# Optimization experiments

Hardware: AMD Instinct MI355X
Metric: run time of the kernel (lower is better)

Reference implementation:

```python
import jax, jax.numpy as jnp
import numpy as np

OUT_FEATURES = 16384
IN_FEATURES = 4096


def setup_inputs() -> dict:
    key = jax.random.key(0)
    k1, k2, k3, k4 = jax.random.split(key, 4)
    # activations [B, S, in]
    x = jax.random.normal(k1, (4, 2048, IN_FEATURES), dtype=jnp.float32)
    # packed int4 weights: two nibbles per uint8, total out*in values (even, no pad)
    n_packed = OUT_FEATURES * IN_FEATURES // 2
    weight_packed = jax.random.randint(k2, (n_packed,), 0, 256, dtype=jnp.int32).astype(jnp.uint8)
    # per-row dequant scale [out, 1], positive like abs-max/7
    scale = jax.random.uniform(k3, (OUT_FEATURES, 1), dtype=jnp.float32, minval=1e-3, maxval=0.05)
    bias = jax.random.normal(k4, (OUT_FEATURES,), dtype=jnp.float32) * 0.01
    return {"x": x, "weight_packed": weight_packed, "scale": scale, "bias": bias}


def reference(x, weight_packed, scale, bias):
    # unpack: even positions = low nibble, odd positions = high nibble
    low = (weight_packed & 15).astype(jnp.int8)
    high = ((weight_packed >> 4) & 15).astype(jnp.int8)
    q = jnp.stack([low, high], axis=-1).reshape(-1)  # interleave -> [out*in]
    # sign-extend 4-bit two's complement: values >7 map to negative
    q = jnp.where(q > 7, q - 16, q)
    # dequantize with per-row scale -> [out, in]
    w = q.reshape(OUT_FEATURES, IN_FEATURES).astype(jnp.float32) * scale
    # F.linear: y = x @ w.T + bias
    return jnp.einsum('bsi,oi->bso', x, w) + bias
```

## Files before the change

### kernel.cpp

```cpp
#include <hip/hip_runtime.h>
#include <hip/hip_bf16.h>
#include <stdint.h>

typedef short short8 __attribute__((ext_vector_type(8)));
typedef float floatx4 __attribute__((ext_vector_type(4)));

static constexpr int KTOT = 4096;
static constexpr int NTOT = 16384;
static constexpr int MTOT = 8192;

#define GLOAD_LDS16(g, l)                                              \
  __builtin_amdgcn_global_load_lds(                                    \
      (const __attribute__((address_space(1))) void*)(g),              \
      (__attribute__((address_space(3))) void*)(l), 16, 0, 0)

__device__ __forceinline__ uint32_t pack2_bf16_rne(float lo, float hi) {
  uint32_t a = __builtin_bit_cast(uint32_t, lo);
  uint32_t b = __builtin_bit_cast(uint32_t, hi);
  a += 0x7FFFu + ((a >> 16) & 1u);
  b += 0x7FFFu + ((b >> 16) & 1u);
  return __builtin_amdgcn_perm(b, a, 0x07060302u);
}


__global__ __launch_bounds__(256) void cvt_x_kernel(
    const float* __restrict__ X, ushort* __restrict__ Xb) {
  const size_t i = (size_t)blockIdx.x * 256 + threadIdx.x;
  const float4 a = *reinterpret_cast<const float4*>(X + i * 8);
  const float4 b = *reinterpret_cast<const float4*>(X + i * 8 + 4);
  uint4 o;
  o.x = pack2_bf16_rne(a.x, a.y);
  o.y = pack2_bf16_rne(a.z, a.w);
  o.z = pack2_bf16_rne(b.x, b.y);
  o.w = pack2_bf16_rne(b.z, b.w);
  *reinterpret_cast<uint4*>(Xb + i * 8) = o;
}

__global__ __launch_bounds__(256) void cvt_w_kernel(
    const uint32_t* __restrict__ Wp, ushort* __restrict__ Wb) {
  const size_t i = (size_t)blockIdx.x * 256 + threadIdx.x;
  const uint4 w = *reinterpret_cast<const uint4*>(Wp + i * 4);
  const uint32_t wd[4] = {w.x, w.y, w.z, w.w};
  uint4 o;
  uint32_t* op = reinterpret_cast<uint32_t*>(&o);
  #pragma unroll
  for (int p = 0; p < 4; ++p) {
    int v0 = ((int)(wd[p] << 28)) >> 28;
    int v1 = ((int)(wd[p] << 24)) >> 28;
    uint32_t f0 = __builtin_bit_cast(uint32_t, (float)v0);
    uint32_t f1 = __builtin_bit_cast(uint32_t, (float)v1);
    op[p] = __builtin_amdgcn_perm(f1, f0, 0x07060302u);
  }
  *reinterpret_cast<uint4*>(Wb + i * 8) = o;
}


static constexpr int BM = 256, BN = 256, BK = 32;
static constexpr int NT = KTOT / BK;

#define READ_FRAGS(AF0, AF1, BF, buf)                                   \
  {                                                                     \
    const ushort* Ab_ = As + (buf) * 8192 + abase + laneoff;            \
    const ushort* Bb_ = Bs + (buf) * 8192 + bbase + laneoff;            \
    _Pragma("unroll")                                                   \
    for (int n = 0; n < 4; ++n)                                         \
      BF[n] = *reinterpret_cast<const short8*>(Bb_ + n * 512);          \
    _Pragma("unroll")                                                   \
    for (int m = 0; m < 4; ++m)                                         \
      AF0[m] = *reinterpret_cast<const short8*>(Ab_ + m * 512);         \
    _Pragma("unroll")                                                   \
    for (int m = 0; m < 4; ++m)                                         \
      AF1[m] = *reinterpret_cast<const short8*>(Ab_ + (m + 4) * 512);   \
  }

#define STAGE(st_)                                                      \
  if ((st_) < NT) {                                                     \
    const int sb_ = (st_) & 3;                                          \
    const size_t kof_ = (size_t)(st_) * BK;                             \
    GLOAD_LDS16(agA + kof_,           aldsw + sb_ * 8192);              \
    GLOAD_LDS16(agA + kof_ + rowstep, aldsw + sb_ * 8192 + 4096);       \
    GLOAD_LDS16(agB + kof_,           bldsw + sb_ * 8192);              \
    GLOAD_LDS16(agB + kof_ + rowstep, bldsw + sb_ * 8192 + 4096);       \
  }

#define MFMA_CLUSTER(AF0, AF1, BF)                                      \
  __builtin_amdgcn_s_setprio(1);                                        \
  _Pragma("unroll")                                                     \
  for (int m = 0; m < 4; ++m)                                           \
    _Pragma("unroll")                                                   \
    for (int n = 0; n < 4; ++n)                                         \
      acc[m][n] = __builtin_amdgcn_mfma_f32_16x16x32_bf16(AF0[m], BF[n], acc[m][n], 0, 0, 0); \
  _Pragma("unroll")                                                     \
  for (int m = 0; m < 4; ++m)                                           \
    _Pragma("unroll")                                                   \
    for (int n = 0; n < 4; ++n)                                         \
      acc[m + 4][n] = __builtin_amdgcn_mfma_f32_16x16x32_bf16(AF1[m], BF[n], acc[m + 4][n], 0, 0, 0); \
  __builtin_amdgcn_s_setprio(0);

#define BOUNDARY(k_)                                                    \
  if ((k_) + 3 < NT) { asm volatile("s_waitcnt vmcnt(4)\ns_barrier" ::: "memory"); } \
  else               { asm volatile("s_waitcnt vmcnt(0)\ns_barrier" ::: "memory"); }

__global__ __launch_bounds__(512, 2) void gemm_bf16_256_kernel(
    const ushort* __restrict__ Xb,
    const ushort* __restrict__ Wb,
    const float* __restrict__ scale,
    const float* __restrict__ bias,
    float* __restrict__ Y)
{
  __shared__ ushort As[4 * 8192];
  __shared__ ushort Bs[4 * 8192];

  const int t    = threadIdx.x;
  const int lane = t & 63;
  const int wv   = t >> 6;
  const int wr   = wv >> 2;
  const int wcn  = wv & 3;

  const int wg  = blockIdx.x;
  const int xcd = wg & 7;
  const int s   = wg >> 3;
  const int bm0 = (xcd * 4 + (s & 3)) * BM;
  const int bn0 = (s >> 2) * BN;

  const int clg  = (t & 7) ^ ((t >> 3) & 7);
  const int srow = ((t >> 3) << 1) | (clg >> 2);
  const int scol = (clg & 3) * 8;
  const ushort* agA = Xb + (size_t)(bm0 + srow) * KTOT + scol;
  const ushort* agB = Wb + (size_t)(bn0 + srow) * KTOT + scol;
  const size_t rowstep = (size_t)128 * KTOT;
  ushort* aldsw = As + wv * 512;
  ushort* bldsw = Bs + wv * 512;

  const int p    = lane >> 4;
  const int l15  = lane & 15;
  const int cph  = (((l15 & 1) << 2) | p) ^ ((l15 >> 1) & 7);
  const int laneoff = (l15 >> 1) * 64 + cph * 8;
  const int abase = wr * 4096;
  const int bbase = wcn * 2048;

  floatx4 acc[8][4];
  #pragma unroll
  for (int m = 0; m < 8; ++m)
    #pragma unroll
    for (int n = 0; n < 4; ++n)
      acc[m][n] = (floatx4){0.f, 0.f, 0.f, 0.f};

  #pragma unroll
  for (int pt = 0; pt < 3; ++pt) {
    const size_t kof = (size_t)pt * BK;
    GLOAD_LDS16(agA + kof,           aldsw + pt * 8192);
    GLOAD_LDS16(agA + kof + rowstep, aldsw + pt * 8192 + 4096);
    GLOAD_LDS16(agB + kof,           bldsw + pt * 8192);
    GLOAD_LDS16(agB + kof + rowstep, bldsw + pt * 8192 + 4096);
  }
  asm volatile("s_waitcnt vmcnt(4)\ns_barrier" ::: "memory");

  short8 a0A[4], a1A[4], bA[4];
  short8 a0B[4], a1B[4], bB[4];
  READ_FRAGS(a0A, a1A, bA, 0);

  for (int kt = 0; kt < NT; kt += 2) {
    READ_FRAGS(a0B, a1B, bB, (kt + 1) & 3);
    STAGE(kt + 3);
    MFMA_CLUSTER(a0A, a1A, bA);
    BOUNDARY(kt);

    if (kt + 2 < NT) { READ_FRAGS(a0A, a1A, bA, (kt + 2) & 3); }
    STAGE(kt + 4);
    MFMA_CLUSTER(a0B, a1B, bB);
    if (kt + 2 < NT) { BOUNDARY(kt + 1); }
  }

  const int crow = (lane >> 4) * 4;
  const int ccol = lane & 15;
  #pragma unroll
  for (int n = 0; n < 4; ++n) {
    const int col  = bn0 + wcn * 64 + n * 16 + ccol;
    const float sc = scale[col];
    const float bz = bias[col];
    #pragma unroll
    for (int m = 0; m < 8; ++m) {
      const int row0 = bm0 + wr * 128 + m * 16 + crow;
      float* yp = Y + (size_t)row0 * NTOT + col;
      #pragma unroll
      for (int r = 0; r < 4; ++r)
        yp[(size_t)r * NTOT] = acc[m][n][r] * sc + bz;
    }
  }
}


static constexpr int FBM = 128, FBN = 128, FBK = 64;
static constexpr int LDSS = 72;
static constexpr int FNSTEP = KTOT / FBK;

__global__ __launch_bounds__(256) void int4_linear_fused_kernel(
    const float* __restrict__ X,
    const uint32_t* __restrict__ Wp,
    const float* __restrict__ scale,
    const float* __restrict__ bias,
    float* __restrict__ Y)
{
  __shared__ ushort As[FBM * LDSS];
  __shared__ ushort Bs[FBN * LDSS];

  const int t    = threadIdx.x;
  const int lane = t & 63;
  const int wv   = t >> 6;
  const int wr   = wv >> 1;
  const int wc   = wv & 1;
  const int bm0 = blockIdx.y * FBM;
  const int bn0 = blockIdx.x * FBN;
  const int srow = t >> 1;
  const int sh   = t & 1;

  const float*    ag = X  + (size_t)(bm0 + srow) * KTOT + sh * 32;
  const uint32_t* bg = Wp + (size_t)(bn0 + srow) * (KTOT / 2) + sh * 16;

  float4 areg[8];
  uint4  breg[4];
  #pragma unroll
  for (int j = 0; j < 8; ++j) areg[j] = *reinterpret_cast<const float4*>(ag + j * 4);
  #pragma unroll
  for (int j = 0; j < 4; ++j) breg[j] = *reinterpret_cast<const uint4*>(bg + j * 4);

  floatx4 acc[4][4];
  #pragma unroll
  for (int m = 0; m < 4; ++m)
    #pragma unroll
    for (int n = 0; n < 4; ++n)
      acc[m][n] = (floatx4){0.f, 0.f, 0.f, 0.f};

  ushort* adst = &As[srow * LDSS + sh * 32];
  ushort* bdst = &Bs[srow * LDSS + sh * 32];

  for (int ks = 0; ks < FNSTEP; ++ks) {
    {
      uint32_t ab[16];
      #pragma unroll
      for (int j = 0; j < 8; ++j) {
        uint32_t u0 = __builtin_bit_cast(uint32_t, areg[j].x) + 0x8000u;
        uint32_t u1 = __builtin_bit_cast(uint32_t, areg[j].y) + 0x8000u;
        uint32_t u2 = __builtin_bit_cast(uint32_t, areg[j].z) + 0x8000u;
        uint32_t u3 = __builtin_bit_cast(uint32_t, areg[j].w) + 0x8000u;
        ab[2*j]   = __builtin_amdgcn_perm(u1, u0, 0x07060302u);
        ab[2*j+1] = __builtin_amdgcn_perm(u3, u2, 0x07060302u);
      }
      uint32_t bb[16];
      #pragma unroll
      for (int j = 0; j < 4; ++j) {
        const uint32_t wq[4] = {breg[j].x, breg[j].y, breg[j].z, breg[j].w};
        #pragma unroll
        for (int p2 = 0; p2 < 4; ++p2) {
          const uint32_t w = wq[p2];
          int v0 = ((int)(w << 28)) >> 28;
          int v1 = ((int)(w << 24)) >> 28;
          uint32_t f0 = __builtin_bit_cast(uint32_t, (float)v0);
          uint32_t f1 = __builtin_bit_cast(uint32_t, (float)v1);
          bb[j*4 + p2] = __builtin_amdgcn_perm(f1, f0, 0x07060302u);
        }
      }
      #pragma unroll
      for (int j = 0; j < 4; ++j) {
        *reinterpret_cast<uint4*>(adst + j * 8) = *reinterpret_cast<const uint4*>(&ab[j*4]);
        *reinterpret_cast<uint4*>(bdst + j * 8) = *reinterpret_cast<const uint4*>(&bb[j*4]);
      }
    }
    __syncthreads();

    if (ks + 1 < FNSTEP) {
      const float*    ap = ag + (ks + 1) * FBK;
      const uint32_t* bp = bg + (ks + 1) * (FBK / 2);
      #pragma unroll
      for (int j = 0; j < 8; ++j) areg[j] = *reinterpret_cast<const float4*>(ap + j * 4);
      #pragma unroll
      for (int j = 0; j < 4; ++j) breg[j] = *reinterpret_cast<const uint4*>(bp + j * 4);
    }

    #pragma unroll
    for (int kk = 0; kk < 2; ++kk) {
      const int ko = kk * 32 + (lane >> 4) * 8;
      short8 af[4], bf[4];
      #pragma unroll
      for (int m = 0; m < 4; ++m)
        af[m] = *reinterpret_cast<const short8*>(&As[(wr*64 + m*16 + (lane & 15)) * LDSS + ko]);
      #pragma unroll
      for (int n = 0; n < 4; ++n)
        bf[n] = *reinterpret_cast<const short8*>(&Bs[(wc*64 + n*16 + (lane & 15)) * LDSS + ko]);
      #pragma unroll
      for (int m = 0; m < 4; ++m)
        #pragma unroll
        for (int n = 0; n < 4; ++n)
          acc[m][n] = __builtin_amdgcn_mfma_f32_16x16x32_bf16(af[m], bf[n], acc[m][n], 0, 0, 0);
    }
    __syncthreads();
  }

  const int crow = (lane >> 4) * 4;
  const int ccol = lane & 15;
  #pragma unroll
  for (int n = 0; n < 4; ++n) {
    const int col  = bn0 + wc * 64 + n * 16 + ccol;
    const float sv = scale[col];
    const float bz = bias[col];
    #pragma unroll
    for (int m = 0; m < 4; ++m) {
      const int row0 = bm0 + wr * 64 + m * 16 + crow;
      float* yp = Y + (size_t)row0 * NTOT + col;
      #pragma unroll
      for (int r = 0; r < 4; ++r)
        yp[(size_t)r * NTOT] = acc[m][n][r] * sv + bz;
    }
  }
}


extern "C" void kernel_launch(void* const* d_in, const int* in_sizes, int n_in,
                              void* d_out, int out_size, void* d_ws, size_t ws_size,
                              hipStream_t stream) {
  (void)in_sizes; (void)n_in; (void)out_size;
  const float*    X     = (const float*)d_in[0];
  const uint32_t* Wp    = (const uint32_t*)d_in[1];
  const float*    scale = (const float*)d_in[2];
  const float*    bias  = (const float*)d_in[3];
  float*          Y     = (float*)d_out;

  const size_t xb_bytes = (size_t)MTOT * KTOT * 2;
  const size_t wb_bytes = (size_t)NTOT * KTOT * 2;
  if (ws_size >= xb_bytes + wb_bytes) {
    ushort* Xb = (ushort*)d_ws;
    ushort* Wb = (ushort*)((char*)d_ws + xb_bytes);
    cvt_x_kernel<<<(MTOT * KTOT) / (8 * 256), 256, 0, stream>>>(X, Xb);
    cvt_w_kernel<<<(NTOT * KTOT / 2) / (4 * 256), 256, 0, stream>>>(Wp, Wb);
    gemm_bf16_256_kernel<<<(MTOT / BM) * (NTOT / BN), 512, 0, stream>>>(Xb, Wb, scale, bias, Y);
  } else {
    dim3 grid(NTOT / FBN, MTOT / FBM);
    int4_linear_fused_kernel<<<grid, 256, 0, stream>>>(X, Wp, scale, bias, Y);
  }
}
```

Measured before the change: 1.083 ms.

## Load weight fragments directly from global into registers, bypassing LDS

B (weight) fragments are now read from global memory straight into registers per wave, instead of being staged through LDS with global_load_lds. This halves LDS usage and the LDS read traffic for B. The cost is that each B element is now fetched once per wave row rather than once per block, so global/L2 traffic for W doubles across the two wave rows. Register loads also have only one tile of prefetch distance, which leaves less latency hiding. The vmcnt waits are adjusted to account for the extra outstanding loads.

Result: slower. 1.673 ms (+54.6%).

```diff
diff --git a/kernel.cpp b/kernel.cpp
--- a/kernel.cpp
+++ b/kernel.cpp
@@ -58,13 +58,9 @@
 static constexpr int BM = 256, BN = 256, BK = 32;
 static constexpr int NT = KTOT / BK;
 
-#define READ_FRAGS(AF0, AF1, BF, buf)                                   \
+#define READ_A(AF0, AF1, buf)                                           \
   {                                                                     \
     const ushort* Ab_ = As + (buf) * 8192 + abase + laneoff;            \
-    const ushort* Bb_ = Bs + (buf) * 8192 + bbase + laneoff;            \
-    _Pragma("unroll")                                                   \
-    for (int n = 0; n < 4; ++n)                                         \
-      BF[n] = *reinterpret_cast<const short8*>(Bb_ + n * 512);          \
     _Pragma("unroll")                                                   \
     for (int m = 0; m < 4; ++m)                                         \
       AF0[m] = *reinterpret_cast<const short8*>(Ab_ + m * 512);         \
@@ -73,14 +69,21 @@
       AF1[m] = *reinterpret_cast<const short8*>(Ab_ + (m + 4) * 512);   \
   }
 
-#define STAGE(st_)                                                      \
+#define LOAD_B(BF, tile_)                                               \
+  {                                                                     \
+    const ushort* b_ = bgl + (size_t)(tile_) * BK;                      \
+    BF[0] = *reinterpret_cast<const short8*>(b_);                       \
+    BF[1] = *reinterpret_cast<const short8*>(b_ + (size_t)16 * KTOT);   \
+    BF[2] = *reinterpret_cast<const short8*>(b_ + (size_t)32 * KTOT);   \
+    BF[3] = *reinterpret_cast<const short8*>(b_ + (size_t)48 * KTOT);   \
+  }
+
+#define STAGE_A(st_)                                                    \
   if ((st_) < NT) {                                                     \
     const int sb_ = (st_) & 3;                                          \
     const size_t kof_ = (size_t)(st_) * BK;                             \
     GLOAD_LDS16(agA + kof_,           aldsw + sb_ * 8192);              \
     GLOAD_LDS16(agA + kof_ + rowstep, aldsw + sb_ * 8192 + 4096);       \
-    GLOAD_LDS16(agB + kof_,           bldsw + sb_ * 8192);              \
-    GLOAD_LDS16(agB + kof_ + rowstep, bldsw + sb_ * 8192 + 4096);       \
   }
 
 #define MFMA_CLUSTER(AF0, AF1, BF)                                      \
@@ -98,8 +101,8 @@
   __builtin_amdgcn_s_setprio(0);
 
 #define BOUNDARY(k_)                                                    \
-  if ((k_) + 3 < NT) { asm volatile("s_waitcnt vmcnt(4)\ns_barrier" ::: "memory"); } \
-  else               { asm volatile("s_waitcnt vmcnt(0)\ns_barrier" ::: "memory"); }
+  if ((k_) + 3 < NT) { asm volatile("s_waitcnt vmcnt(6)\ns_barrier" ::: "memory"); } \
+  else               { asm volatile("s_waitcnt vmcnt(4)\ns_barrier" ::: "memory"); }
 
 __global__ __launch_bounds__(512, 2) void gemm_bf16_256_kernel(
     const ushort* __restrict__ Xb,
@@ -109,7 +112,6 @@
     float* __restrict__ Y)
 {
   __shared__ ushort As[4 * 8192];
-  __shared__ ushort Bs[4 * 8192];
 
   const int t    = threadIdx.x;
   const int lane = t & 63;
@@ -127,17 +129,16 @@
   const int srow = ((t >> 3) << 1) | (clg >> 2);
   const int scol = (clg & 3) * 8;
   const ushort* agA = Xb + (size_t)(bm0 + srow) * KTOT + scol;
-  const ushort* agB = Wb + (size_t)(bn0 + srow) * KTOT + scol;
   const size_t rowstep = (size_t)128 * KTOT;
   ushort* aldsw = As + wv * 512;
-  ushort* bldsw = Bs + wv * 512;
 
   const int p    = lane >> 4;
   const int l15  = lane & 15;
   const int cph  = (((l15 & 1) << 2) | p) ^ ((l15 >> 1) & 7);
   const int laneoff = (l15 >> 1) * 64 + cph * 8;
   const int abase = wr * 4096;
-  const int bbase = wcn * 2048;
+
+  const ushort* bgl = Wb + (size_t)(bn0 + wcn * 64 + l15) * KTOT + p * 8;
 
   floatx4 acc[8][4];
   #pragma unroll
@@ -151,23 +152,23 @@
     const size_t kof = (size_t)pt * BK;
     GLOAD_LDS16(agA + kof,           aldsw + pt * 8192);
     GLOAD_LDS16(agA + kof + rowstep, aldsw + pt * 8192 + 4096);
-    GLOAD_LDS16(agB + kof,           bldsw + pt * 8192);
-    GLOAD_LDS16(agB + kof + rowstep, bldsw + pt * 8192 + 4096);
-  }
-  asm volatile("s_waitcnt vmcnt(4)\ns_barrier" ::: "memory");
+  }
+  asm volatile("s_waitcnt vmcnt(2)\ns_barrier" ::: "memory");
 
   short8 a0A[4], a1A[4], bA[4];
   short8 a0B[4], a1B[4], bB[4];
-  READ_FRAGS(a0A, a1A, bA, 0);
+  READ_A(a0A, a1A, 0);
+  LOAD_B(bA, 0);
 
   for (int kt = 0; kt < NT; kt += 2) {
-    READ_FRAGS(a0B, a1B, bB, (kt + 1) & 3);
-    STAGE(kt + 3);
+    READ_A(a0B, a1B, (kt + 1) & 3);
+    LOAD_B(bB, kt + 1);
+    STAGE_A(kt + 3);
     MFMA_CLUSTER(a0A, a1A, bA);
     BOUNDARY(kt);
 
-    if (kt + 2 < NT) { READ_FRAGS(a0A, a1A, bA, (kt + 2) & 3); }
-    STAGE(kt + 4);
+    if (kt + 2 < NT) { READ_A(a0A, a1A, (kt + 2) & 3); LOAD_B(bA, kt + 2); }
+    STAGE_A(kt + 4);
     MFMA_CLUSTER(a0B, a1B, bB);
     if (kt + 2 < NT) { BOUNDARY(kt + 1); }
   }
```
